# Kernel optimization log

Measured on AMD Instinct MI355X. Metric: run time of the kernel, lower is better.

Reference implementation:

```python
import jax, jax.numpy as jnp
import numpy as np

B, N, IN_DIM, OUT_DIM, H = 8, 1024, 256, 256, 8
D = OUT_DIM // H  # head_dim = 32
NEG_INF = -1.0e9


def setup_inputs() -> dict:
    key = jax.random.key(0)
    k_x, k_adj, k_W, k_a = jax.random.split(key, 4)
    x = jax.random.normal(k_x, (B, N, IN_DIM), dtype=jnp.float32)
    adj = jax.random.randint(k_adj, (B, N, N), 0, 2, dtype=jnp.int32)
    # nn.Linear(in_dim, out_dim, bias=False): weight [out_dim, in_dim]
    lim = 1.0 / np.sqrt(IN_DIM)
    W = jax.random.uniform(k_W, (OUT_DIM, IN_DIM), jnp.float32, -lim, lim)
    # a: (1, H, 2*D), xavier_uniform with gain=1.414
    gain = 1.414
    bound = gain * np.sqrt(6.0 / (H + 2 * D))
    a = jax.random.uniform(k_a, (1, H, 2 * D), jnp.float32, -bound, bound)
    return {"x": x, "adj": adj, "W": W, "a": a}


def reference(x, adj, W, a):
    Bn, Nn, _ = x.shape
    h = jnp.einsum('bni,oi->bno', x, W).reshape(Bn, Nn, H, D)  # [B,N,H,D]
    # sum(cat(h_i, h_j) * a) = h_i . a_src + h_j . a_dst  (avoids O(N^2*2D) concat)
    a_src = a[0, :, :D]   # [H,D] multiplies h_i (query/row index i)
    a_dst = a[0, :, D:]   # [H,D] multiplies h_j (key/col index j)
    s_i = jnp.einsum('bnhd,hd->bnh', h, a_src)  # [B,N,H]
    s_j = jnp.einsum('bnhd,hd->bnh', h, a_dst)  # [B,N,H]
    e = s_i[:, :, None, :] + s_j[:, None, :, :]  # [B,i,j,H]
    e = jnp.where(e > 0, e, 0.2 * e)  # LeakyReLU(0.2)
    mask = (adj != 0)[..., None]      # [B,N,N,1] broadcast over heads
    e = jnp.where(mask, e, NEG_INF)
    alpha = jax.nn.softmax(e, axis=2)  # softmax over j (neighbors)
    # dropout p=0.0 -> identity
    h_prime = jnp.einsum('bijh,bjhd->bihd', alpha, h)
    h_prime = h_prime.reshape(Bn, Nn, H * D)
    return jax.nn.elu(h_prime)
```

## Files before the change

kernel.cpp:

```cpp
#include <hip/hip_runtime.h>
#include <cmath>

namespace {
constexpr int B = 8, N = 1024, IND = 256, OUTD = 256, H = 8, D = 32;
constexpr float LOG2E = 1.4426950408889634f;
}

typedef __attribute__((ext_vector_type(8))) short short8v;
typedef __attribute__((ext_vector_type(4))) float f32x4;

__device__ inline ushort f2bf(float f) {
  __bf16 b = (__bf16)f;
  return __builtin_bit_cast(ushort, b);
}
__device__ inline float bf2f(ushort u) {
  return __uint_as_float((uint)u << 16);
}

__global__ __launch_bounds__(256) void gat_k1(
    const float* __restrict__ x, const float* __restrict__ W,
    const float* __restrict__ a, const int* __restrict__ adj,
    uint* __restrict__ bitsT, float* __restrict__ siT,
    float* __restrict__ sjT, ushort* __restrict__ hTbF) {
  const int bid = blockIdx.x;
  const int t = threadIdx.x;

  if (bid >= 512) {
    const int lane = t & 63, w = t >> 6;
    const int wid = (bid - 512) * 4 + w;
    const int b = wid >> 10, i = wid & 1023;
    const int4* ap = (const int4*)(adj + ((size_t)b * N + i) * N);
#pragma unroll
    for (int c = 0; c < 4; ++c) {
      const int4 v = ap[c * 64 + lane];
      uint val = (v.x != 0 ? 1u : 0u) | (v.y != 0 ? 2u : 0u) |
                 (v.z != 0 ? 4u : 0u) | (v.w != 0 ? 8u : 0u);
      val <<= (lane & 7) * 4;
      val |= (uint)__shfl_xor((int)val, 1);
      val |= (uint)__shfl_xor((int)val, 2);
      val |= (uint)__shfl_xor((int)val, 4);
      if ((lane & 7) == 0) {
        const int jt = c * 8 + (lane >> 3);
        bitsT[((size_t)b * 32 + jt) * N + i] = val;
      }
    }
    return;
  }

  __shared__ __align__(16) char smem[17664];
  float(*xs)[36] = (float(*)[36])smem;
  ushort* wsh = (ushort*)(smem + 9216);
  ushort* wsl = (ushort*)(smem + 13312);
  float(*tile2)[65] = (float(*)[65])smem;

  const int lane = t & 63, w = t >> 6;
  const int la = lane & 15, g = lane >> 4;
  const int work = ((bid & 7) << 6) + (bid >> 3);
  const int bx = work >> 2, by = work & 3;

  f32x4 z = {0.f, 0.f, 0.f, 0.f};
  f32x4 acc[4] = {z, z, z, z};

  const float* xp = x + (size_t)(bx * 64 + (t >> 2)) * IND + (t & 3) * 8;
  const int w_c = by * 64 + (t >> 6) * 16 + (t & 15);
  const int w_k0 = ((t >> 4) & 3) * 8;
  const float* wp = W + (size_t)w_c * IND + w_k0;

  for (int kb = 0; kb < 8; ++kb) {
    __syncthreads();
    {
      float4 v0 = *(const float4*)(xp + kb * 32);
      float4 v1 = *(const float4*)(xp + kb * 32 + 4);
      float* dst = &xs[t >> 2][(t & 3) * 8];
      *(float4*)dst = v0;
      *(float4*)(dst + 4) = v1;
    }
    {
      float4 v0 = *(const float4*)(wp + kb * 32);
      float4 v1 = *(const float4*)(wp + kb * 32 + 4);
      const float wf[8] = {v0.x, v0.y, v0.z, v0.w, v1.x, v1.y, v1.z, v1.w};
      short8v ph, pl;
#pragma unroll
      for (int e = 0; e < 8; ++e) {
        const ushort hi = f2bf(wf[e]);
        ph[e] = (short)hi;
        pl[e] = (short)f2bf(wf[e] - bf2f(hi));
      }
      *(short8v*)&wsh[t * 8] = ph;
      *(short8v*)&wsl[t * 8] = pl;
    }
    __syncthreads();

    const float* xr = &xs[w * 16 + la][g * 8];
    float4 u0 = *(const float4*)(xr);
    float4 u1 = *(const float4*)(xr + 4);
    const float af[8] = {u0.x, u0.y, u0.z, u0.w, u1.x, u1.y, u1.z, u1.w};
    short8v ah, al;
#pragma unroll
    for (int e = 0; e < 8; ++e) {
      const ushort hb = f2bf(af[e]);
      ah[e] = (short)hb;
      al[e] = (short)f2bf(af[e] - bf2f(hb));
    }
#pragma unroll
    for (int ct = 0; ct < 4; ++ct) {
      const short8v bh = *(const short8v*)&wsh[ct * 512 + lane * 8];
      const short8v bl = *(const short8v*)&wsl[ct * 512 + lane * 8];
      acc[ct] = __builtin_amdgcn_mfma_f32_16x16x32_bf16(ah, bh, acc[ct], 0, 0, 0);
      acc[ct] = __builtin_amdgcn_mfma_f32_16x16x32_bf16(al, bh, acc[ct], 0, 0, 0);
      acc[ct] = __builtin_amdgcn_mfma_f32_16x16x32_bf16(ah, bl, acc[ct], 0, 0, 0);
    }
  }

  const int batch = bx >> 4;
  const int nbase = (bx & 15) * 64 + w * 16;

#pragma unroll
  for (int hp2 = 0; hp2 < 2; ++hp2) {
    const int head = by * 2 + hp2;
    const float a0 = a[head * 64 + la] * LOG2E;
    const float a1 = a[head * 64 + 16 + la] * LOG2E;
    const float a2 = a[head * 64 + 32 + la] * LOG2E;
    const float a3 = a[head * 64 + 48 + la] * LOG2E;
    float s1v[4], s2v[4];
#pragma unroll
    for (int q = 0; q < 4; ++q) {
      s1v[q] = acc[hp2 * 2][q] * a0 + acc[hp2 * 2 + 1][q] * a1;
      s2v[q] = acc[hp2 * 2][q] * a2 + acc[hp2 * 2 + 1][q] * a3;
    }
#pragma unroll
    for (int mask = 1; mask <= 8; mask <<= 1)
#pragma unroll
      for (int q = 0; q < 4; ++q) {
        s1v[q] += __shfl_xor(s1v[q], mask);
        s2v[q] += __shfl_xor(s2v[q], mask);
      }
    if (la == 0) {
#pragma unroll
      for (int q = 0; q < 4; ++q) {
        const size_t o = (size_t)(batch * H + head) * N + nbase + g * 4 + q;
        siT[o] = s1v[q];
        sjT[o] = s2v[q];
      }
    }
  }

  __syncthreads();
#pragma unroll
  for (int ct = 0; ct < 4; ++ct)
#pragma unroll
    for (int q = 0; q < 4; ++q)
      tile2[w * 16 + g * 4 + q][ct * 16 + la] = acc[ct][q];
  __syncthreads();

  const int jt0 = (bx & 15) * 2;
#pragma unroll
  for (int s = 0; s < 2; ++s) {
    const int gg = t * 2 + s;
    const int head = gg >> 8, rem = gg & 255;
    const int jt_loc = rem >> 7, half = (rem >> 6) & 1, l = rem & 63;
    const int d = half * 16 + (l & 15);
    short8v pk;
#pragma unroll
    for (int e = 0; e < 8; ++e)
      pk[e] = (short)f2bf(tile2[jt_loc * 32 + (l >> 4) * 8 + e][head * 32 + d]);
    const int bh_g = batch * H + by * 2 + head;
    *(short8v*)(hTbF + ((size_t)(bh_g * 32 + jt0 + jt_loc) * 64 + l) * 16 + half * 8) = pk;
  }
}

__global__ __launch_bounds__(256) void gat_agg(
    const uint* __restrict__ bitsT, const float* __restrict__ siT,
    const float* __restrict__ sjT, const ushort* __restrict__ hTbF,
    float* __restrict__ out) {
  __shared__ float part[2][64][13];
  const int t = threadIdx.x;
  const int lane = t & 63, w = t >> 6;
  const int iw = w & 1, jq = w >> 1;
  const int bid = blockIdx.x;
  const int work = ((bid & 7) << 8) + (bid >> 3);
  const int bh = work >> 5;
  const int itg = work & 31;
  const int b = bh >> 3, hh = bh & 7;
  const int i0 = itg * 32 + iw * 16;
  const int la = lane & 15, g = lane >> 4;
  const int iA = i0 + la;

  const float si_r = siT[(size_t)bh * N + iA];
  const uint* btp = bitsT + (size_t)b * 32 * N + (size_t)jq * 16 * N + iA;
  const float* sjp = sjT + (size_t)bh * N + jq * 512 + g * 8;
  const ushort* hp = hTbF + (size_t)bh * 32768 + (size_t)jq * 16384 + lane * 16;

  f32x4 acc0 = {0.f, 0.f, 0.f, 0.f}, acc1 = {0.f, 0.f, 0.f, 0.f};
  f32x4 accl = {0.f, 0.f, 0.f, 0.f};
  short8v ones;
#pragma unroll
  for (int e = 0; e < 8; ++e) ones[e] = (short)0x3F80;

  uint bits0, bits1;
  float4 sjA0, sjB0, sjA1, sjB1;
  short8v b00, b10, b01, b11;

#define AGG_LOAD(S, JT)                                      \
  bits##S = btp[(size_t)(JT)*1024];                          \
  sjA##S = *(const float4*)(sjp + (JT) * 32);                \
  sjB##S = *(const float4*)(sjp + (JT) * 32 + 4);            \
  b0##S = *(const short8v*)(hp + (size_t)(JT)*1024);         \
  b1##S = *(const short8v*)(hp + (size_t)(JT)*1024 + 8);

#define AGG_COMP(S)                                                           \
  {                                                                           \
    const uint byte_ = (bits##S >> (g * 8)) & 0xffu;                          \
    const float sjv[8] = {sjA##S.x, sjA##S.y, sjA##S.z, sjA##S.w,             \
                          sjB##S.x, sjB##S.y, sjB##S.z, sjB##S.w};            \
    short8v af;                                                               \
    _Pragma("unroll") for (int e = 0; e < 8; ++e) {                           \
      float s = si_r + sjv[e];                                                \
      s = fmaxf(s, 0.2f * s);                                                 \
      s = ((byte_ >> e) & 1u) ? s : -INFINITY;                                \
      af[e] = (short)f2bf(__builtin_amdgcn_exp2f(s));                         \
    }                                                                         \
    __builtin_amdgcn_s_setprio(1);                                            \
    acc0 = __builtin_amdgcn_mfma_f32_16x16x32_bf16(af, b0##S, acc0, 0, 0, 0); \
    acc1 = __builtin_amdgcn_mfma_f32_16x16x32_bf16(af, b1##S, acc1, 0, 0, 0); \
    accl = __builtin_amdgcn_mfma_f32_16x16x32_bf16(af, ones, accl, 0, 0, 0);  \
    __builtin_amdgcn_s_setprio(0);                                            \
  }

  AGG_LOAD(0, 0)
  AGG_LOAD(1, 1)
#pragma unroll
  for (int jt = 0; jt < 16; jt += 2) {
    AGG_COMP(0)
    if (jt + 2 < 16) { AGG_LOAD(0, jt + 2) }
    AGG_COMP(1)
    if (jt + 3 < 16) { AGG_LOAD(1, jt + 3) }
  }
#undef AGG_LOAD
#undef AGG_COMP

  if (jq == 1) {
    float* p = part[iw][lane];
#pragma unroll
    for (int k = 0; k < 4; ++k) {
      p[k] = acc0[k];
      p[4 + k] = acc1[k];
      p[8 + k] = accl[k];
    }
  }
  __syncthreads();
  if (jq == 0) {
    const float* p = part[iw][lane];
#pragma unroll
    for (int k = 0; k < 4; ++k) {
      acc0[k] += p[k];
      acc1[k] += p[4 + k];
      accl[k] += p[8 + k];
    }
    float* op = out + ((size_t)(b * N + i0)) * OUTD + hh * D;
#pragma unroll
    for (int r = 0; r < 4; ++r) {
      const int ic = g * 4 + r;
      const float li = accl[r];
      float v0 = acc0[r] / li;
      v0 = v0 > 0.f ? v0 : expm1f(v0);
      op[(size_t)ic * OUTD + la] = v0;
      float v1 = acc1[r] / li;
      v1 = v1 > 0.f ? v1 : expm1f(v1);
      op[(size_t)ic * OUTD + 16 + la] = v1;
    }
  }
}

extern "C" void kernel_launch(void* const* d_in, const int* in_sizes, int n_in,
                              void* d_out, int out_size, void* d_ws, size_t ws_size,
                              hipStream_t stream) {
  const float* x = (const float*)d_in[0];
  const int* adj = (const int*)d_in[1];
  const float* W = (const float*)d_in[2];
  const float* a = (const float*)d_in[3];
  float* out = (float*)d_out;

  float* ws = (float*)d_ws;
  float* siT = ws;
  float* sjT = siT + (size_t)B * N * H;
  uint* bitsT = (uint*)(sjT + (size_t)B * N * H);
  ushort* hTbF = (ushort*)(bitsT + (size_t)B * 32 * N);

  gat_k1<<<512 + 2048, 256, 0, stream>>>(x, W, a, adj, bitsT, siT, sjT, hTbF);
  gat_agg<<<2048, 256, 0, stream>>>(bitsT, siT, sjT, hTbF, out);
}
```

Before: 42.11 us.

## Process 64 query rows per block with 4-way j-split in GAT aggregation

Restructures the aggregation kernel so each block handles 64 query rows (four 16-row MFMA groups per wave) and splits the neighbor dimension four ways across waves instead of two, halving the grid. The h and sj tiles loaded per j-step are reused across four row groups, which cuts redundant global loads of the value matrix. In exchange it raises register pressure (twelve accumulators per wave), uses a larger shared-memory reduction, and gives fewer blocks, which may lower occupancy and latency hiding.

```diff
diff --git a/kernel.cpp b/kernel.cpp
--- a/kernel.cpp
+++ b/kernel.cpp
@@ -173,102 +173,140 @@
     const uint* __restrict__ bitsT, const float* __restrict__ siT,
     const float* __restrict__ sjT, const ushort* __restrict__ hTbF,
     float* __restrict__ out) {
-  __shared__ float part[2][64][13];
+  __shared__ float part[3][64][49];
   const int t = threadIdx.x;
-  const int lane = t & 63, w = t >> 6;
-  const int iw = w & 1, jq = w >> 1;
+  const int lane = t & 63, jq = t >> 6;
   const int bid = blockIdx.x;
-  const int work = ((bid & 7) << 8) + (bid >> 3);
-  const int bh = work >> 5;
-  const int itg = work & 31;
+  const int work = ((bid & 7) << 7) + (bid >> 3);
+  const int bh = work >> 4;
+  const int itg = work & 15;
   const int b = bh >> 3, hh = bh & 7;
-  const int i0 = itg * 32 + iw * 16;
+  const int i0 = itg * 64;
   const int la = lane & 15, g = lane >> 4;
-  const int iA = i0 + la;
-
-  const float si_r = siT[(size_t)bh * N + iA];
-  const uint* btp = bitsT + (size_t)b * 32 * N + (size_t)jq * 16 * N + iA;
-  const float* sjp = sjT + (size_t)bh * N + jq * 512 + g * 8;
-  const ushort* hp = hTbF + (size_t)bh * 32768 + (size_t)jq * 16384 + lane * 16;
-
-  f32x4 acc0 = {0.f, 0.f, 0.f, 0.f}, acc1 = {0.f, 0.f, 0.f, 0.f};
-  f32x4 accl = {0.f, 0.f, 0.f, 0.f};
+
+  const float si_0 = siT[(size_t)bh * N + i0 + la];
+  const float si_1 = siT[(size_t)bh * N + i0 + 16 + la];
+  const float si_2 = siT[(size_t)bh * N + i0 + 32 + la];
+  const float si_3 = siT[(size_t)bh * N + i0 + 48 + la];
+
+  const uint* btp = bitsT + (size_t)b * 32 * N + (size_t)jq * 8 * N + i0 + la;
+  const float* sjp = sjT + (size_t)bh * N + jq * 256 + g * 8;
+  const ushort* hp = hTbF + (size_t)bh * 32768 + (size_t)jq * 8192 + lane * 16;
+
+  f32x4 z = {0.f, 0.f, 0.f, 0.f};
+  f32x4 c0_0 = z, c1_0 = z, cl_0 = z;
+  f32x4 c0_1 = z, c1_1 = z, cl_1 = z;
+  f32x4 c0_2 = z, c1_2 = z, cl_2 = z;
+  f32x4 c0_3 = z, c1_3 = z, cl_3 = z;
   short8v ones;
 #pragma unroll
   for (int e = 0; e < 8; ++e) ones[e] = (short)0x3F80;
 
-  uint bits0, bits1;
-  float4 sjA0, sjB0, sjA1, sjB1;
-  short8v b00, b10, b01, b11;
-
-#define AGG_LOAD(S, JT)                                      \
-  bits##S = btp[(size_t)(JT)*1024];                          \
-  sjA##S = *(const float4*)(sjp + (JT) * 32);                \
-  sjB##S = *(const float4*)(sjp + (JT) * 32 + 4);            \
-  b0##S = *(const short8v*)(hp + (size_t)(JT)*1024);         \
-  b1##S = *(const short8v*)(hp + (size_t)(JT)*1024 + 8);
-
-#define AGG_COMP(S)                                                           \
-  {                                                                           \
-    const uint byte_ = (bits##S >> (g * 8)) & 0xffu;                          \
-    const float sjv[8] = {sjA##S.x, sjA##S.y, sjA##S.z, sjA##S.w,             \
-                          sjB##S.x, sjB##S.y, sjB##S.z, sjB##S.w};            \
-    short8v af;                                                               \
-    _Pragma("unroll") for (int e = 0; e < 8; ++e) {                           \
-      float s = si_r + sjv[e];                                                \
-      s = fmaxf(s, 0.2f * s);                                                 \
-      s = ((byte_ >> e) & 1u) ? s : -INFINITY;                                \
-      af[e] = (short)f2bf(__builtin_amdgcn_exp2f(s));                         \
-    }                                                                         \
-    __builtin_amdgcn_s_setprio(1);                                            \
-    acc0 = __builtin_amdgcn_mfma_f32_16x16x32_bf16(af, b0##S, acc0, 0, 0, 0); \
-    acc1 = __builtin_amdgcn_mfma_f32_16x16x32_bf16(af, b1##S, acc1, 0, 0, 0); \
-    accl = __builtin_amdgcn_mfma_f32_16x16x32_bf16(af, ones, accl, 0, 0, 0);  \
-    __builtin_amdgcn_s_setprio(0);                                            \
-  }
-
-  AGG_LOAD(0, 0)
-  AGG_LOAD(1, 1)
-#pragma unroll
-  for (int jt = 0; jt < 16; jt += 2) {
-    AGG_COMP(0)
-    if (jt + 2 < 16) { AGG_LOAD(0, jt + 2) }
-    AGG_COMP(1)
-    if (jt + 3 < 16) { AGG_LOAD(1, jt + 3) }
+  uint bA_0, bA_1, bA_2, bA_3, bB_0, bB_1, bB_2, bB_3;
+  float4 sjAA, sjBA, sjAB, sjBB;
+  short8v h0A, h1A, h0B, h1B;
+
+#define AGG_LOAD(S, JT)                                   \
+  b##S##_0 = btp[(size_t)(JT)*1024];                      \
+  b##S##_1 = btp[(size_t)(JT)*1024 + 16];                 \
+  b##S##_2 = btp[(size_t)(JT)*1024 + 32];                 \
+  b##S##_3 = btp[(size_t)(JT)*1024 + 48];                 \
+  sjA##S = *(const float4*)(sjp + (JT) * 32);             \
+  sjB##S = *(const float4*)(sjp + (JT) * 32 + 4);         \
+  h0##S = *(const short8v*)(hp + (size_t)(JT)*1024);      \
+  h1##S = *(const short8v*)(hp + (size_t)(JT)*1024 + 8);
+
+#define MK_AF(AF, BITS, SI)                               \
+  {                                                       \
+    const uint byte_ = ((BITS) >> (g * 8)) & 0xffu;       \
+    _Pragma("unroll") for (int e = 0; e < 8; ++e) {       \
+      float s = (SI) + sjv[e];                            \
+      s = fmaxf(s, 0.2f * s);                             \
+      s = ((byte_ >> e) & 1u) ? s : -INFINITY;            \
+      AF[e] = (short)f2bf(__builtin_amdgcn_exp2f(s));     \
+    }                                                     \
+  }
+
+#define AGG_COMP(S)                                                            \
+  {                                                                            \
+    const float sjv[8] = {sjA##S.x, sjA##S.y, sjA##S.z, sjA##S.w,              \
+                          sjB##S.x, sjB##S.y, sjB##S.z, sjB##S.w};             \
+    short8v af0, af1, af2, af3;                                                \
+    MK_AF(af0, b##S##_0, si_0)                                                 \
+    MK_AF(af1, b##S##_1, si_1)                                                 \
+    MK_AF(af2, b##S##_2, si_2)                                                 \
+    MK_AF(af3, b##S##_3, si_3)                                                 \
+    __builtin_amdgcn_s_setprio(1);                                             \
+    c0_0 = __builtin_amdgcn_mfma_f32_16x16x32_bf16(af0, h0##S, c0_0, 0, 0, 0); \
+    c1_0 = __builtin_amdgcn_mfma_f32_16x16x32_bf16(af0, h1##S, c1_0, 0, 0, 0); \
+    cl_0 = __builtin_amdgcn_mfma_f32_16x16x32_bf16(af0, ones, cl_0, 0, 0, 0);  \
+    c0_1 = __builtin_amdgcn_mfma_f32_16x16x32_bf16(af1, h0##S, c0_1, 0, 0, 0); \
+    c1_1 = __builtin_amdgcn_mfma_f32_16x16x32_bf16(af1, h1##S, c1_1, 0, 0, 0); \
+    cl_1 = __builtin_amdgcn_mfma_f32_16x16x32_bf16(af1, ones, cl_1, 0, 0, 0);  \
+    c0_2 = __builtin_amdgcn_mfma_f32_16x16x32_bf16(af2, h0##S, c0_2, 0, 0, 0); \
+    c1_2 = __builtin_amdgcn_mfma_f32_16x16x32_bf16(af2, h1##S, c1_2, 0, 0, 0); \
+    cl_2 = __builtin_amdgcn_mfma_f32_16x16x32_bf16(af2, ones, cl_2, 0, 0, 0);  \
+    c0_3 = __builtin_amdgcn_mfma_f32_16x16x32_bf16(af3, h0##S, c0_3, 0, 0, 0); \
+    c1_3 = __builtin_amdgcn_mfma_f32_16x16x32_bf16(af3, h1##S, c1_3, 0, 0, 0); \
+    cl_3 = __builtin_amdgcn_mfma_f32_16x16x32_bf16(af3, ones, cl_3, 0, 0, 0);  \
+    __builtin_amdgcn_s_setprio(0);                                             \
+  }
+
+  AGG_LOAD(A, 0)
+  AGG_LOAD(B, 1)
+#pragma unroll
+  for (int jt = 0; jt < 8; jt += 2) {
+    AGG_COMP(A)
+    if (jt + 2 < 8) { AGG_LOAD(A, jt + 2) }
+    AGG_COMP(B)
+    if (jt + 3 < 8) { AGG_LOAD(B, jt + 3) }
   }
 #undef AGG_LOAD
+#undef MK_AF
 #undef AGG_COMP
 
-  if (jq == 1) {
-    float* p = part[iw][lane];
+  if (jq != 0) {
+    float* p = part[jq - 1][lane];
 #pragma unroll
     for (int k = 0; k < 4; ++k) {
-      p[k] = acc0[k];
-      p[4 + k] = acc1[k];
-      p[8 + k] = accl[k];
+      p[k] = c0_0[k];      p[4 + k] = c1_0[k];  p[8 + k] = cl_0[k];
+      p[12 + k] = c0_1[k]; p[16 + k] = c1_1[k]; p[20 + k] = cl_1[k];
+      p[24 + k] = c0_2[k]; p[28 + k] = c1_2[k]; p[32 + k] = cl_2[k];
+      p[36 + k] = c0_3[k]; p[40 + k] = c1_3[k]; p[44 + k] = cl_3[k];
     }
   }
   __syncthreads();
   if (jq == 0) {
-    const float* p = part[iw][lane];
-#pragma unroll
-    for (int k = 0; k < 4; ++k) {
-      acc0[k] += p[k];
-      acc1[k] += p[4 + k];
-      accl[k] += p[8 + k];
-    }
-    float* op = out + ((size_t)(b * N + i0)) * OUTD + hh * D;
-#pragma unroll
-    for (int r = 0; r < 4; ++r) {
-      const int ic = g * 4 + r;
-      const float li = accl[r];
-      float v0 = acc0[r] / li;
-      v0 = v0 > 0.f ? v0 : expm1f(v0);
-      op[(size_t)ic * OUTD + la] = v0;
-      float v1 = acc1[r] / li;
-      v1 = v1 > 0.f ? v1 : expm1f(v1);
-      op[(size_t)ic * OUTD + 16 + la] = v1;
-    }
+#pragma unroll
+    for (int q = 0; q < 3; ++q) {
+      const float* p = part[q][lane];
+#pragma unroll
+      for (int k = 0; k < 4; ++k) {
+        c0_0[k] += p[k];      c1_0[k] += p[4 + k];  cl_0[k] += p[8 + k];
+        c0_1[k] += p[12 + k]; c1_1[k] += p[16 + k]; cl_1[k] += p[20 + k];
+        c0_2[k] += p[24 + k]; c1_2[k] += p[28 + k]; cl_2[k] += p[32 + k];
+        c0_3[k] += p[36 + k]; c1_3[k] += p[40 + k]; cl_3[k] += p[44 + k];
+      }
+    }
+#define EPI(GR, C0, C1, CL)                                                  \
+    {                                                                        \
+      float* op = out + ((size_t)(b * N + i0 + (GR)*16)) * OUTD + hh * D;    \
+      _Pragma("unroll") for (int r = 0; r < 4; ++r) {                        \
+        const int ic = g * 4 + r;                                            \
+        const float li = CL[r];                                              \
+        float v0 = C0[r] / li;                                               \
+        v0 = v0 > 0.f ? v0 : expm1f(v0);                                     \
+        op[(size_t)ic * OUTD + la] = v0;                                     \
+        float v1 = C1[r] / li;                                               \
+        v1 = v1 > 0.f ? v1 : expm1f(v1);                                     \
+        op[(size_t)ic * OUTD + 16 + la] = v1;                                \
+      }                                                                      \
+    }
+    EPI(0, c0_0, c1_0, cl_0)
+    EPI(1, c0_1, c1_1, cl_1)
+    EPI(2, c0_2, c1_2, cl_2)
+    EPI(3, c0_3, c1_3, cl_3)
+#undef EPI
   }
 }
 
@@ -288,5 +326,5 @@
   ushort* hTbF = (ushort*)(bitsT + (size_t)B * 32 * N);
 
   gat_k1<<<512 + 2048, 256, 0, stream>>>(x, W, a, adj, bitsT, siT, sjT, hTbF);
-  gat_agg<<<2048, 256, 0, stream>>>(bitsT, siT, sjT, hTbF, out);
-}
+  gat_agg<<<1024, 256, 0, stream>>>(bitsT, siT, sjT, hTbF, out);
+}
```

Result: slower. 62.26 us (+47.8%).
